# Kernel tuning notes

Measured on AMD Instinct MI355X. Metric: run time of the kernel, lower is better.

The kernel has to match this reference:

```python
import jax, jax.numpy as jnp
import numpy as np

N = 100000
E = 1600000
D_IN = 128
D_HID = 128
D_OUT = 128
HEADS = 4
NEG_SLOPE = 0.2  # PyG GATConv default leaky_relu slope


def setup_inputs() -> dict:
    key = jax.random.key(0)
    ks = jax.random.split(key, 16)
    ch1 = D_HID // HEADS
    ch2 = D_OUT // HEADS
    inp = {
        "x": jax.random.normal(ks[0], (N, D_IN), dtype=jnp.float32),
        "edge_index": jax.random.randint(ks[1], (2, E), 0, N, dtype=jnp.int64),
        # conv1 params
        "W1": jax.random.normal(ks[2], (D_IN, HEADS * ch1), dtype=jnp.float32) * 0.05,
        "a1_src": jax.random.normal(ks[3], (HEADS, ch1), dtype=jnp.float32) * 0.05,
        "a1_dst": jax.random.normal(ks[4], (HEADS, ch1), dtype=jnp.float32) * 0.05,
        "b1": jnp.zeros((HEADS * ch1,), dtype=jnp.float32),
        # conv2 params
        "W2": jax.random.normal(ks[5], (D_HID, HEADS * ch2), dtype=jnp.float32) * 0.05,
        "a2_src": jax.random.normal(ks[6], (HEADS, ch2), dtype=jnp.float32) * 0.05,
        "a2_dst": jax.random.normal(ks[7], (HEADS, ch2), dtype=jnp.float32) * 0.05,
        "b2": jnp.zeros((HEADS * ch2,), dtype=jnp.float32),
        # residual linear
        "Wr": jax.random.normal(ks[8], (D_IN, D_OUT), dtype=jnp.float32) * 0.05,
        "br": jnp.zeros((D_OUT,), dtype=jnp.float32),
    }
    return inp


def _gat_conv(x, W, a_src, a_dst, bias, src, dst, n_nodes):
    """Single PyG-style GATConv (concat heads, eval-mode / no dropout).
    src/dst already include self loops. x: [N, Din]. Returns [N, H*C]."""
    H, C = a_src.shape
    h = (x @ W).reshape(n_nodes, H, C)                      # [N,H,C]
    s_src = jnp.einsum("nhc,hc->nh", h, a_src)              # [N,H]
    s_dst = jnp.einsum("nhc,hc->nh", h, a_dst)              # [N,H]
    e = s_src[src] + s_dst[dst]                             # [E',H]
    e = jnp.where(e > 0, e, NEG_SLOPE * e)                  # leaky_relu
    # softmax over edges grouped by destination node
    e_max = jax.ops.segment_max(e, dst, num_segments=n_nodes)  # [N,H]
    e_exp = jnp.exp(e - e_max[dst])
    denom = jax.ops.segment_sum(e_exp, dst, num_segments=n_nodes)  # [N,H]
    alpha = e_exp / denom[dst]                              # [E',H]
    msg = alpha[:, :, None] * h[src]                        # [E',H,C]
    out = jax.ops.segment_sum(msg, dst, num_segments=n_nodes)  # [N,H,C]
    return out.reshape(n_nodes, H * C) + bias


def reference(x, edge_index, W1, a1_src, a1_dst, b1, W2, a2_src, a2_dst, b2, Wr, br):
    n_nodes = x.shape[0]
    loops = jnp.arange(n_nodes, dtype=edge_index.dtype)
    src = jnp.concatenate([edge_index[0], loops])           # add_self_loops=True
    dst = jnp.concatenate([edge_index[1], loops])
    h1 = _gat_conv(x, W1, a1_src, a1_dst, b1, src, dst, n_nodes)
    h1 = jax.nn.relu(h1)
    h2 = _gat_conv(h1, W2, a2_src, a2_dst, b2, src, dst, n_nodes)
    return h2 + x @ Wr + br
```

## Files before the change

### kernel.cpp

```cpp
#include <hip/hip_runtime.h>

#define NEG_SLOPE 0.2f

__device__ __forceinline__ float leaky1(float e) { return e > 0.f ? e : NEG_SLOPE * e; }

__device__ __forceinline__ unsigned short f2bf(float f) {
    unsigned u = __float_as_uint(f);
    u += 0x7fffu + ((u >> 16) & 1u);
    return (unsigned short)(u >> 16);
}

#define EPB 4096

__global__ __launch_bounds__(256) void bucket_hist(const int* __restrict__ dst,
                                                   int* __restrict__ gcnt,
                                                   int* __restrict__ relBase,
                                                   int E, int N, int NB) {
    __shared__ int hist[256];
    int t = threadIdx.x, blk = blockIdx.x;
    if (t < NB) hist[t] = 0;
    __syncthreads();
    int e0 = blk * EPB + t;
#pragma unroll 4
    for (int k = 0; k < EPB / 256; ++k) {
        int e = e0 + k * 256;
        if (e < E) {
            int d = dst[e];
            if ((unsigned)d < (unsigned)N) atomicAdd(&hist[d >> 9], 1);
        }
    }
    __syncthreads();
    if (t < NB) relBase[blk * NB + t] = atomicAdd(&gcnt[t], hist[t]);
}

__global__ __launch_bounds__(256) void scan_buckets(const int* __restrict__ gcnt,
                                                    int* __restrict__ gboff, int NB) {
    __shared__ int sm[256];
    int t = threadIdx.x;
    int v = (t < NB) ? gcnt[t] : 0;
    sm[t] = v;
    __syncthreads();
#pragma unroll
    for (int o = 1; o < 256; o <<= 1) {
        int u = (t >= o) ? sm[t - o] : 0;
        __syncthreads();
        sm[t] += u;
        __syncthreads();
    }
    if (t < NB) gboff[t] = sm[t] - v;
    if (t == NB - 1) gboff[NB] = sm[t];
}

__global__ __launch_bounds__(256) void bucket_scatter(const int* __restrict__ src,
                                                      const int* __restrict__ dst,
                                                      const int* __restrict__ gboff,
                                                      const int* __restrict__ relBase,
                                                      int2* __restrict__ eb,
                                                      int E, int N, int NB) {
    __shared__ int cur[256];
    int t = threadIdx.x, blk = blockIdx.x;
    if (t < NB) cur[t] = gboff[t] + relBase[blk * NB + t];
    __syncthreads();
    int e0 = blk * EPB + t;
#pragma unroll 4
    for (int k = 0; k < EPB / 256; ++k) {
        int e = e0 + k * 256;
        if (e < E) {
            int d = dst[e];
            if ((unsigned)d < (unsigned)N) {
                int pos = atomicAdd(&cur[d >> 9], 1);
                eb[pos] = make_int2(src[e], d);
            }
        }
    }
}

__global__ __launch_bounds__(512) void csr_build(const int2* __restrict__ eb,
                                                 const int* __restrict__ gboff,
                                                 int* __restrict__ offs,
                                                 int* __restrict__ csr,
                                                 int N, int NB) {
    __shared__ int lcnt[512];
    __shared__ int sm[512];
    __shared__ int cur[512];
    int t = threadIdx.x, b = blockIdx.x;
    lcnt[t] = 0;
    __syncthreads();
    int s0 = gboff[b], s1 = gboff[b + 1];
    for (int e = s0 + t; e < s1; e += 512) atomicAdd(&lcnt[eb[e].y & 511], 1);
    __syncthreads();
    int v = lcnt[t];
    sm[t] = v;
    __syncthreads();
#pragma unroll
    for (int o = 1; o < 512; o <<= 1) {
        int u = (t >= o) ? sm[t - o] : 0;
        __syncthreads();
        sm[t] += u;
        __syncthreads();
    }
    int base = gboff[b] + sm[t] - v;
    cur[t] = base;
    int n0 = (b << 9) + t;
    if (n0 < N) offs[n0] = base;
    if (b == NB - 1 && t == 0) offs[N] = gboff[NB];
    __syncthreads();
    for (int e = s0 + t; e < s1; e += 512) {
        int2 p = eb[e];
        int pos = atomicAdd(&cur[p.y & 511], 1);
        csr[pos] = p.x;
    }
}


__global__ __launch_bounds__(256) void gemm128(const float* __restrict__ X,
                                               const float* __restrict__ W,
                                               float* __restrict__ OUT,
                                               unsigned short* __restrict__ HB,
                                               const float* __restrict__ bias,
                                               int accumulate,
                                               const float* __restrict__ ASrc,
                                               const float* __restrict__ ADst,
                                               float* __restrict__ sSt,
                                               float* __restrict__ sDt, int N) {
    __shared__ float Xs[32][128];
    __shared__ float Ws[64][128];
    int t = threadIdx.x;
    int row0 = blockIdx.x << 5;
    {
        const float4* xg = (const float4*)(X + (size_t)row0 * 128);
        float4* xs = (float4*)&Xs[0][0];
#pragma unroll
        for (int i = 0; i < 4; ++i) xs[t + 256 * i] = xg[t + 256 * i];
    }
    int cx = t & 31, ry = t >> 5;
    int c0 = cx << 2, r0 = ry << 2;
    float acc[4][4] = {};
#pragma unroll 1
    for (int ph = 0; ph < 2; ++ph) {
        __syncthreads();
        {
            const float4* wg = (const float4*)(W + (size_t)ph * 64 * 128);
            float4* ws = (float4*)&Ws[0][0];
#pragma unroll
            for (int i = 0; i < 8; ++i) ws[t + 256 * i] = wg[t + 256 * i];
        }
        __syncthreads();
#pragma unroll 4
        for (int k4 = 0; k4 < 16; ++k4) {
            float4 a[4], b[4];
#pragma unroll
            for (int i = 0; i < 4; ++i)
                a[i] = *(const float4*)&Xs[r0 + i][(ph << 6) + (k4 << 2)];
#pragma unroll
            for (int kk = 0; kk < 4; ++kk)
                b[kk] = *(const float4*)&Ws[(k4 << 2) + kk][c0];
#pragma unroll
            for (int i = 0; i < 4; ++i) {
                acc[i][0] = fmaf(a[i].x, b[0].x, acc[i][0]);
                acc[i][1] = fmaf(a[i].x, b[0].y, acc[i][1]);
                acc[i][2] = fmaf(a[i].x, b[0].z, acc[i][2]);
                acc[i][3] = fmaf(a[i].x, b[0].w, acc[i][3]);
                acc[i][0] = fmaf(a[i].y, b[1].x, acc[i][0]);
                acc[i][1] = fmaf(a[i].y, b[1].y, acc[i][1]);
                acc[i][2] = fmaf(a[i].y, b[1].z, acc[i][2]);
                acc[i][3] = fmaf(a[i].y, b[1].w, acc[i][3]);
                acc[i][0] = fmaf(a[i].z, b[2].x, acc[i][0]);
                acc[i][1] = fmaf(a[i].z, b[2].y, acc[i][1]);
                acc[i][2] = fmaf(a[i].z, b[2].z, acc[i][2]);
                acc[i][3] = fmaf(a[i].z, b[2].w, acc[i][3]);
                acc[i][0] = fmaf(a[i].w, b[3].x, acc[i][0]);
                acc[i][1] = fmaf(a[i].w, b[3].y, acc[i][1]);
                acc[i][2] = fmaf(a[i].w, b[3].z, acc[i][2]);
                acc[i][3] = fmaf(a[i].w, b[3].w, acc[i][3]);
            }
        }
    }
    float4 bv = make_float4(0.f, 0.f, 0.f, 0.f);
    if (bias) bv = *(const float4*)&bias[c0];
    float4 sa = make_float4(0.f, 0.f, 0.f, 0.f), da = sa;
    if (ASrc) {
        sa = *(const float4*)&ASrc[c0];
        da = *(const float4*)&ADst[c0];
    }
#pragma unroll
    for (int i = 0; i < 4; ++i) {
        size_t row = (size_t)(row0 + r0 + i);
        float4 o;
        o.x = acc[i][0] + bv.x;
        o.y = acc[i][1] + bv.y;
        o.z = acc[i][2] + bv.z;
        o.w = acc[i][3] + bv.w;
        if (accumulate) {
            const float4 old = *(const float4*)(OUT + row * 128 + c0);
            o.x += old.x; o.y += old.y; o.z += old.z; o.w += old.w;
        }
        if (OUT) *(float4*)(OUT + row * 128 + c0) = o;
        if (HB) {
            ushort4 hv;
            hv.x = f2bf(o.x); hv.y = f2bf(o.y); hv.z = f2bf(o.z); hv.w = f2bf(o.w);
            *(ushort4*)(HB + row * 128 + c0) = hv;
        }
        if (ASrc) {
            float ps = o.x * sa.x + o.y * sa.y + o.z * sa.z + o.w * sa.w;
            float pd = o.x * da.x + o.y * da.y + o.z * da.z + o.w * da.w;
            ps += __shfl_xor(ps, 1); pd += __shfl_xor(pd, 1);
            ps += __shfl_xor(ps, 2); pd += __shfl_xor(pd, 2);
            ps += __shfl_xor(ps, 4); pd += __shfl_xor(pd, 4);
            if ((cx & 7) == 0) {
                size_t sidx = (size_t)(cx >> 3) * N + row;
                sSt[sidx] = ps;
                sDt[sidx] = pd;
            }
        }
    }
}


__global__ __launch_bounds__(256) void agg5_kernel(const unsigned short* __restrict__ hb,
                                                   const float* __restrict__ sSt,
                                                   const float* __restrict__ sDt,
                                                   const int* __restrict__ offs,
                                                   const int* __restrict__ csr,
                                                   const float* __restrict__ bias,
                                                   float* __restrict__ out,
                                                   int do_relu, int N) {
    int n = (blockIdx.x << 2) + (threadIdx.x >> 6);
    if (n >= N) return;
    int lane = threadIdx.x & 63;
    int half = lane >> 5;
    int cl = lane & 31;
    int hd = cl >> 3;
    int whead = lane >> 4;
    int sub = lane & 15;

    size_t wb = (size_t)whead * N;
    float sdh = sDt[wb + n];
    float selfw = __expf(leaky1(sSt[wb + n] + sdh));

    float4 acc = make_float4(0.f, 0.f, 0.f, 0.f);
    float wsum = 0.f;

    int off = offs[n], end = offs[n + 1];
    for (int base = off; base < end; base += 64) {
        int idx = base + lane;
        int spre = (idx < end) ? csr[idx] : 0;
        int cnt = min(64, end - base);
#pragma unroll 1
        for (int lo = 0; lo < cnt; lo += 16) {
            float w = 0.f;
            {
                int s2 = __shfl(spre, lo + sub);
                if (lo + sub < cnt) w = __expf(leaky1(sSt[wb + s2] + sdh));
            }
            wsum += w;
#pragma unroll
            for (int i = 0; i < 16; i += 2) {
                int sj = __shfl(spre, lo + i + half);
                float wj = __shfl(w, (hd << 4) + i + half);
                uint2 v = *(const uint2*)(hb + (size_t)sj * 128 + 4 * cl);
                acc.x = fmaf(wj, __uint_as_float(v.x << 16), acc.x);
                acc.y = fmaf(wj, __uint_as_float(v.x & 0xffff0000u), acc.y);
                acc.z = fmaf(wj, __uint_as_float(v.y << 16), acc.z);
                acc.w = fmaf(wj, __uint_as_float(v.y & 0xffff0000u), acc.w);
            }
        }
    }
    acc.x += __shfl_xor(acc.x, 32);
    acc.y += __shfl_xor(acc.y, 32);
    acc.z += __shfl_xor(acc.z, 32);
    acc.w += __shfl_xor(acc.w, 32);
#pragma unroll
    for (int o = 8; o > 0; o >>= 1) wsum += __shfl_xor(wsum, o);
    float denom = wsum + selfw;
    float iv = 1.0f / __shfl(denom, hd << 4);
    float sw = __shfl(selfw, hd << 4);

    if (half == 0) {
        uint2 hv = *(const uint2*)(hb + (size_t)n * 128 + 4 * cl);
        float4 hs;
        hs.x = __uint_as_float(hv.x << 16);
        hs.y = __uint_as_float(hv.x & 0xffff0000u);
        hs.z = __uint_as_float(hv.y << 16);
        hs.w = __uint_as_float(hv.y & 0xffff0000u);
        float4 bvv = *(const float4*)(bias + 4 * cl);
        float4 o;
        o.x = fmaf(fmaf(sw, hs.x, acc.x), iv, bvv.x);
        o.y = fmaf(fmaf(sw, hs.y, acc.y), iv, bvv.y);
        o.z = fmaf(fmaf(sw, hs.z, acc.z), iv, bvv.z);
        o.w = fmaf(fmaf(sw, hs.w, acc.w), iv, bvv.w);
        if (do_relu) {
            o.x = fmaxf(o.x, 0.f); o.y = fmaxf(o.y, 0.f);
            o.z = fmaxf(o.z, 0.f); o.w = fmaxf(o.w, 0.f);
        }
        *(float4*)(out + (size_t)n * 128 + 4 * cl) = o;
    }
}


extern "C" void kernel_launch(void* const* d_in, const int* in_sizes, int n_in,
                              void* d_out, int out_size, void* d_ws, size_t ws_size,
                              hipStream_t stream) {
    const float* x   = (const float*)d_in[0];
    const int*   ei  = (const int*)d_in[1];
    const float* W1  = (const float*)d_in[2];
    const float* a1s = (const float*)d_in[3];
    const float* a1d = (const float*)d_in[4];
    const float* b1  = (const float*)d_in[5];
    const float* W2  = (const float*)d_in[6];
    const float* a2s = (const float*)d_in[7];
    const float* a2d = (const float*)d_in[8];
    const float* b2  = (const float*)d_in[9];
    const float* Wr  = (const float*)d_in[10];
    const float* br  = (const float*)d_in[11];
    float* out = (float*)d_out;

    int N = in_sizes[0] / 128;
    int E = in_sizes[1] / 2;
    const int* src = ei;
    const int* dst = ei + E;
    int NB = (N + 511) >> 9;
    int ebl = (E + EPB - 1) / EPB;

    char* w = (char*)d_ws;
    size_t p = 0;
    auto take = [&](size_t bytes) -> char* {
        char* r = w + p;
        p = (p + bytes + 255) & ~(size_t)255;
        return r;
    };
    float* bufB = (float*)take((size_t)N * 128 * 4);
    unsigned short* hb = (unsigned short*)take((size_t)N * 128 * 2);
    float* sSt  = (float*)take((size_t)N * 4 * 4);
    float* sDt  = (float*)take((size_t)N * 4 * 4);
    int* gcnt   = (int*)take((size_t)256 * 4);
    int* offs   = (int*)take((size_t)(N + 1) * 4);
    int* gboff  = (int*)take((size_t)257 * 4);
    int* relBase = (int*)take((size_t)ebl * NB * 4);
    int2* eb    = (int2*)take((size_t)E * 8);
    int* csr    = (int*)take((size_t)E * 4);

    hipMemsetAsync(gcnt, 0, 256 * 4, stream);

    bucket_hist<<<ebl, 256, 0, stream>>>(dst, gcnt, relBase, E, N, NB);
    scan_buckets<<<1, 256, 0, stream>>>(gcnt, gboff, NB);
    bucket_scatter<<<ebl, 256, 0, stream>>>(src, dst, gboff, relBase, eb, E, N, NB);
    csr_build<<<NB, 512, 0, stream>>>(eb, gboff, offs, csr, N, NB);

    int gb = N / 32;
    int ab = (N + 3) / 4;

    gemm128<<<gb, 256, 0, stream>>>(x, W1, nullptr, hb, nullptr, 0, a1s, a1d, sSt, sDt, N);
    agg5_kernel<<<ab, 256, 0, stream>>>(hb, sSt, sDt, offs, csr, b1, bufB, 1, N);
    gemm128<<<gb, 256, 0, stream>>>(bufB, W2, nullptr, hb, nullptr, 0, a2s, a2d, sSt, sDt, N);
    agg5_kernel<<<ab, 256, 0, stream>>>(hb, sSt, sDt, offs, csr, b2, out, 0, N);
    gemm128<<<gb, 256, 0, stream>>>(x, Wr, out, nullptr, br, 1, nullptr, nullptr, nullptr, nullptr, N);
}
```

Before: 487.8 us.

## Use bf16 MFMA GEMMs, pack edge buckets into single ints, split score kernel

Replaces the fp32 FMA GEMM with a bf16 MFMA 16x16x32 kernel that uses pre-transposed bf16 weights produced by a new prep kernel. The attention-score computation moves out of the GEMM epilogue into a separate kernel that reads the bf16 features. Edge bucket entries are packed into one int (src plus local dst in the high bits), which halves the intermediate bucket buffer traffic. The trade-off is bf16 rounding of inputs and of the residual path, scalar uncoalesced epilogue stores, an extra kernel launch per layer, and the packing assumes N fits in 23 bits.

```diff
diff --git a/kernel.cpp b/kernel.cpp
--- a/kernel.cpp
+++ b/kernel.cpp
@@ -1,6 +1,9 @@
 #include <hip/hip_runtime.h>
 
 #define NEG_SLOPE 0.2f
+
+typedef short bf16x8 __attribute__((ext_vector_type(8)));
+typedef float f32x4 __attribute__((ext_vector_type(4)));
 
 __device__ __forceinline__ float leaky1(float e) { return e > 0.f ? e : NEG_SLOPE * e; }
 
@@ -55,7 +58,7 @@
                                                       const int* __restrict__ dst,
                                                       const int* __restrict__ gboff,
                                                       const int* __restrict__ relBase,
-                                                      int2* __restrict__ eb,
+                                                      int* __restrict__ eb,
                                                       int E, int N, int NB) {
     __shared__ int cur[256];
     int t = threadIdx.x, blk = blockIdx.x;
@@ -69,13 +72,13 @@
             int d = dst[e];
             if ((unsigned)d < (unsigned)N) {
                 int pos = atomicAdd(&cur[d >> 9], 1);
-                eb[pos] = make_int2(src[e], d);
+                eb[pos] = src[e] | ((d & 511) << 23);
             }
         }
     }
 }
 
-__global__ __launch_bounds__(512) void csr_build(const int2* __restrict__ eb,
+__global__ __launch_bounds__(512) void csr_build(const int* __restrict__ eb,
                                                  const int* __restrict__ gboff,
                                                  int* __restrict__ offs,
                                                  int* __restrict__ csr,
@@ -87,7 +90,7 @@
     lcnt[t] = 0;
     __syncthreads();
     int s0 = gboff[b], s1 = gboff[b + 1];
-    for (int e = s0 + t; e < s1; e += 512) atomicAdd(&lcnt[eb[e].y & 511], 1);
+    for (int e = s0 + t; e < s1; e += 512) atomicAdd(&lcnt[(unsigned)eb[e] >> 23], 1);
     __syncthreads();
     int v = lcnt[t];
     sm[t] = v;
@@ -106,114 +109,124 @@
     if (b == NB - 1 && t == 0) offs[N] = gboff[NB];
     __syncthreads();
     for (int e = s0 + t; e < s1; e += 512) {
-        int2 p = eb[e];
-        int pos = atomicAdd(&cur[p.y & 511], 1);
-        csr[pos] = p.x;
-    }
-}
-
-
-__global__ __launch_bounds__(256) void gemm128(const float* __restrict__ X,
-                                               const float* __restrict__ W,
-                                               float* __restrict__ OUT,
-                                               unsigned short* __restrict__ HB,
-                                               const float* __restrict__ bias,
-                                               int accumulate,
-                                               const float* __restrict__ ASrc,
-                                               const float* __restrict__ ADst,
-                                               float* __restrict__ sSt,
-                                               float* __restrict__ sDt, int N) {
-    __shared__ float Xs[32][128];
-    __shared__ float Ws[64][128];
+        int p = eb[e];
+        int pos = atomicAdd(&cur[(unsigned)p >> 23], 1);
+        csr[pos] = p & 0x7FFFFF;
+    }
+}
+
+
+__global__ __launch_bounds__(256) void prep_wT(const float* __restrict__ W1,
+                                               const float* __restrict__ W2,
+                                               const float* __restrict__ Wr,
+                                               unsigned short* __restrict__ T1,
+                                               unsigned short* __restrict__ T2,
+                                               unsigned short* __restrict__ Tr) {
+    int b = blockIdx.x, t = threadIdx.x;
+    const float* W = b == 0 ? W1 : b == 1 ? W2 : Wr;
+    unsigned short* O = b == 0 ? T1 : b == 1 ? T2 : Tr;
+#pragma unroll 4
+    for (int i = 0; i < 64; ++i) {
+        int idx = t + 256 * i;
+        int k = idx >> 7, n = idx & 127;
+        O[n * 128 + k] = f2bf(W[k * 128 + n]);
+    }
+}
+
+#define WP 136
+
+__global__ __launch_bounds__(256) void gemm_mfma(const float* __restrict__ X,
+                                                 const unsigned short* __restrict__ WT,
+                                                 float* __restrict__ OUT,
+                                                 unsigned short* __restrict__ HB,
+                                                 const float* __restrict__ bias,
+                                                 int accumulate, int N) {
+    __shared__ unsigned short Xs[64 * WP];
+    __shared__ unsigned short Ws[128 * WP];
     int t = threadIdx.x;
-    int row0 = blockIdx.x << 5;
-    {
-        const float4* xg = (const float4*)(X + (size_t)row0 * 128);
-        float4* xs = (float4*)&Xs[0][0];
-#pragma unroll
-        for (int i = 0; i < 4; ++i) xs[t + 256 * i] = xg[t + 256 * i];
-    }
-    int cx = t & 31, ry = t >> 5;
-    int c0 = cx << 2, r0 = ry << 2;
-    float acc[4][4] = {};
-#pragma unroll 1
-    for (int ph = 0; ph < 2; ++ph) {
-        __syncthreads();
-        {
-            const float4* wg = (const float4*)(W + (size_t)ph * 64 * 128);
-            float4* ws = (float4*)&Ws[0][0];
-#pragma unroll
-            for (int i = 0; i < 8; ++i) ws[t + 256 * i] = wg[t + 256 * i];
-        }
-        __syncthreads();
-#pragma unroll 4
-        for (int k4 = 0; k4 < 16; ++k4) {
-            float4 a[4], b[4];
-#pragma unroll
-            for (int i = 0; i < 4; ++i)
-                a[i] = *(const float4*)&Xs[r0 + i][(ph << 6) + (k4 << 2)];
-#pragma unroll
-            for (int kk = 0; kk < 4; ++kk)
-                b[kk] = *(const float4*)&Ws[(k4 << 2) + kk][c0];
-#pragma unroll
-            for (int i = 0; i < 4; ++i) {
-                acc[i][0] = fmaf(a[i].x, b[0].x, acc[i][0]);
-                acc[i][1] = fmaf(a[i].x, b[0].y, acc[i][1]);
-                acc[i][2] = fmaf(a[i].x, b[0].z, acc[i][2]);
-                acc[i][3] = fmaf(a[i].x, b[0].w, acc[i][3]);
-                acc[i][0] = fmaf(a[i].y, b[1].x, acc[i][0]);
-                acc[i][1] = fmaf(a[i].y, b[1].y, acc[i][1]);
-                acc[i][2] = fmaf(a[i].y, b[1].z, acc[i][2]);
-                acc[i][3] = fmaf(a[i].y, b[1].w, acc[i][3]);
-                acc[i][0] = fmaf(a[i].z, b[2].x, acc[i][0]);
-                acc[i][1] = fmaf(a[i].z, b[2].y, acc[i][1]);
-                acc[i][2] = fmaf(a[i].z, b[2].z, acc[i][2]);
-                acc[i][3] = fmaf(a[i].z, b[2].w, acc[i][3]);
-                acc[i][0] = fmaf(a[i].w, b[3].x, acc[i][0]);
-                acc[i][1] = fmaf(a[i].w, b[3].y, acc[i][1]);
-                acc[i][2] = fmaf(a[i].w, b[3].z, acc[i][2]);
-                acc[i][3] = fmaf(a[i].w, b[3].w, acc[i][3]);
+    int row0 = blockIdx.x << 6;
+#pragma unroll
+    for (int i = 0; i < 8; ++i) {
+        int f = t + 256 * i;
+        int r = f >> 5, c4 = f & 31;
+        float4 v = make_float4(0.f, 0.f, 0.f, 0.f);
+        if (row0 + r < N) v = *(const float4*)(X + (size_t)(row0 + r) * 128 + c4 * 4);
+        ushort4 u;
+        u.x = f2bf(v.x); u.y = f2bf(v.y); u.z = f2bf(v.z); u.w = f2bf(v.w);
+        *(ushort4*)&Xs[r * WP + c4 * 4] = u;
+    }
+#pragma unroll
+    for (int i = 0; i < 8; ++i) {
+        int f = t + 256 * i;
+        int r = f >> 4, c8 = f & 15;
+        *(uint4*)&Ws[r * WP + c8 * 8] = *(const uint4*)(WT + r * 128 + c8 * 8);
+    }
+    __syncthreads();
+
+    int lane = t & 63;
+    int wv = t >> 6;
+    int col = lane & 15, quad = lane >> 4;
+    f32x4 acc[8];
+#pragma unroll
+    for (int ct = 0; ct < 8; ++ct) acc[ct] = (f32x4){0.f, 0.f, 0.f, 0.f};
+#pragma unroll
+    for (int k0 = 0; k0 < 128; k0 += 32) {
+        bf16x8 a = *(const bf16x8*)&Xs[(wv * 16 + col) * WP + k0 + quad * 8];
+#pragma unroll
+        for (int ct = 0; ct < 8; ++ct) {
+            bf16x8 b = *(const bf16x8*)&Ws[(ct * 16 + col) * WP + k0 + quad * 8];
+            acc[ct] = __builtin_amdgcn_mfma_f32_16x16x32_bf16(a, b, acc[ct], 0, 0, 0);
+        }
+    }
+#pragma unroll
+    for (int ct = 0; ct < 8; ++ct) {
+        int c = ct * 16 + col;
+        float bv = bias ? bias[c] : 0.f;
+#pragma unroll
+        for (int reg = 0; reg < 4; ++reg) {
+            int grow = row0 + wv * 16 + quad * 4 + reg;
+            if (grow < N) {
+                float o = acc[ct][reg] + bv;
+                if (OUT) {
+                    if (accumulate) o += OUT[(size_t)grow * 128 + c];
+                    OUT[(size_t)grow * 128 + c] = o;
+                }
+                if (HB) HB[(size_t)grow * 128 + c] = f2bf(o);
             }
         }
     }
-    float4 bv = make_float4(0.f, 0.f, 0.f, 0.f);
-    if (bias) bv = *(const float4*)&bias[c0];
-    float4 sa = make_float4(0.f, 0.f, 0.f, 0.f), da = sa;
-    if (ASrc) {
-        sa = *(const float4*)&ASrc[c0];
-        da = *(const float4*)&ADst[c0];
-    }
-#pragma unroll
-    for (int i = 0; i < 4; ++i) {
-        size_t row = (size_t)(row0 + r0 + i);
-        float4 o;
-        o.x = acc[i][0] + bv.x;
-        o.y = acc[i][1] + bv.y;
-        o.z = acc[i][2] + bv.z;
-        o.w = acc[i][3] + bv.w;
-        if (accumulate) {
-            const float4 old = *(const float4*)(OUT + row * 128 + c0);
-            o.x += old.x; o.y += old.y; o.z += old.z; o.w += old.w;
-        }
-        if (OUT) *(float4*)(OUT + row * 128 + c0) = o;
-        if (HB) {
-            ushort4 hv;
-            hv.x = f2bf(o.x); hv.y = f2bf(o.y); hv.z = f2bf(o.z); hv.w = f2bf(o.w);
-            *(ushort4*)(HB + row * 128 + c0) = hv;
-        }
-        if (ASrc) {
-            float ps = o.x * sa.x + o.y * sa.y + o.z * sa.z + o.w * sa.w;
-            float pd = o.x * da.x + o.y * da.y + o.z * da.z + o.w * da.w;
-            ps += __shfl_xor(ps, 1); pd += __shfl_xor(pd, 1);
-            ps += __shfl_xor(ps, 2); pd += __shfl_xor(pd, 2);
-            ps += __shfl_xor(ps, 4); pd += __shfl_xor(pd, 4);
-            if ((cx & 7) == 0) {
-                size_t sidx = (size_t)(cx >> 3) * N + row;
-                sSt[sidx] = ps;
-                sDt[sidx] = pd;
-            }
-        }
-    }
+}
+
+
+__global__ __launch_bounds__(256) void s_kernel_bf(const unsigned short* __restrict__ hb,
+                                                   const float* __restrict__ a_s,
+                                                   const float* __restrict__ a_d,
+                                                   float* __restrict__ sSt,
+                                                   float* __restrict__ sDt, int N) {
+    int gid = blockIdx.x * 256 + threadIdx.x;
+    if (gid >= N * 4) return;
+    int n = gid >> 2, hd = gid & 3;
+    const uint4* hp = (const uint4*)(hb + (size_t)n * 128 + hd * 32);
+    const float* as = a_s + hd * 32;
+    const float* ad = a_d + hd * 32;
+    float ss = 0.f, sd = 0.f;
+#pragma unroll
+    for (int q = 0; q < 4; ++q) {
+        uint4 v = hp[q];
+        unsigned vv[4] = {v.x, v.y, v.z, v.w};
+#pragma unroll
+        for (int j = 0; j < 4; ++j) {
+            float lo = __uint_as_float(vv[j] << 16);
+            float hi = __uint_as_float(vv[j] & 0xffff0000u);
+            int c = q * 8 + 2 * j;
+            ss = fmaf(lo, as[c], ss);
+            sd = fmaf(lo, ad[c], sd);
+            ss = fmaf(hi, as[c + 1], ss);
+            sd = fmaf(hi, ad[c + 1], sd);
+        }
+    }
+    sSt[(size_t)hd * N + n] = ss;
+    sDt[(size_t)hd * N + n] = sd;
 }
 
 
@@ -331,28 +344,35 @@
     };
     float* bufB = (float*)take((size_t)N * 128 * 4);
     unsigned short* hb = (unsigned short*)take((size_t)N * 128 * 2);
+    unsigned short* wT1 = (unsigned short*)take(128 * 128 * 2);
+    unsigned short* wT2 = (unsigned short*)take(128 * 128 * 2);
+    unsigned short* wTr = (unsigned short*)take(128 * 128 * 2);
     float* sSt  = (float*)take((size_t)N * 4 * 4);
     float* sDt  = (float*)take((size_t)N * 4 * 4);
     int* gcnt   = (int*)take((size_t)256 * 4);
     int* offs   = (int*)take((size_t)(N + 1) * 4);
     int* gboff  = (int*)take((size_t)257 * 4);
     int* relBase = (int*)take((size_t)ebl * NB * 4);
-    int2* eb    = (int2*)take((size_t)E * 8);
+    int* eb     = (int*)take((size_t)E * 4);
     int* csr    = (int*)take((size_t)E * 4);
 
     hipMemsetAsync(gcnt, 0, 256 * 4, stream);
 
+    prep_wT<<<3, 256, 0, stream>>>(W1, W2, Wr, wT1, wT2, wTr);
     bucket_hist<<<ebl, 256, 0, stream>>>(dst, gcnt, relBase, E, N, NB);
     scan_buckets<<<1, 256, 0, stream>>>(gcnt, gboff, NB);
     bucket_scatter<<<ebl, 256, 0, stream>>>(src, dst, gboff, relBase, eb, E, N, NB);
     csr_build<<<NB, 512, 0, stream>>>(eb, gboff, offs, csr, N, NB);
 
-    int gb = N / 32;
+    int gb = (N + 63) / 64;
+    int sb = (N * 4 + 255) / 256;
     int ab = (N + 3) / 4;
 
-    gemm128<<<gb, 256, 0, stream>>>(x, W1, nullptr, hb, nullptr, 0, a1s, a1d, sSt, sDt, N);
+    gemm_mfma<<<gb, 256, 0, stream>>>(x, wT1, nullptr, hb, nullptr, 0, N);
+    s_kernel_bf<<<sb, 256, 0, stream>>>(hb, a1s, a1d, sSt, sDt, N);
     agg5_kernel<<<ab, 256, 0, stream>>>(hb, sSt, sDt, offs, csr, b1, bufB, 1, N);
-    gemm128<<<gb, 256, 0, stream>>>(bufB, W2, nullptr, hb, nullptr, 0, a2s, a2d, sSt, sDt, N);
+    gemm_mfma<<<gb, 256, 0, stream>>>(bufB, wT2, nullptr, hb, nullptr, 0, N);
+    s_kernel_bf<<<sb, 256, 0, stream>>>(hb, a2s, a2d, sSt, sDt, N);
     agg5_kernel<<<ab, 256, 0, stream>>>(hb, sSt, sDt, offs, csr, b2, out, 0, N);
-    gemm128<<<gb, 256, 0, stream>>>(x, Wr, out, nullptr, br, 1, nullptr, nullptr, nullptr, nullptr, N);
-}
+    gemm_mfma<<<gb, 256, 0, stream>>>(x, wTr, out, nullptr, br, 1, N);
+}
```

Result: no change. 493.0 us (+1.1%).
